# Performance work log

Hardware: AMD Instinct MI355X
Metric: run time of the kernel (lower is better)

## Reference

```python
import jax, jax.numpy as jnp
import numpy as np

T, N, G = 4, 100000, 128
R, B, K = 4, 4096, 32
I = 128


def setup_inputs() -> dict:
    key = jax.random.key(0)
    k1, k2, k3, k4 = jax.random.split(key, 4)
    embeddings = jax.random.normal(k1, (T, N, G), dtype=jnp.float32)
    neighbor_idx = jax.random.randint(k2, (T, R, B, K), 0, N, dtype=jnp.int32)
    neighbor_mask = jax.random.randint(k3, (T, R, B, K), 0, 2).astype(jnp.bool_)
    # xavier_uniform per relation weight [G, I]
    limit = float(np.sqrt(6.0 / (G + I)))
    weights = jax.random.uniform(k4, (R, G, I), dtype=jnp.float32, minval=-limit, maxval=limit)
    return {
        "embeddings": embeddings,
        "weights": weights,
        "neighbor_idx": neighbor_idx,
        "neighbor_mask": neighbor_mask,
        "train_year": T,
    }


def reference(embeddings, weights, neighbor_idx, neighbor_mask, train_year):
    # embeddings: [T, N, G]; neighbor_idx/mask: [T, R, B, K]; weights: [R, G, I]
    m = neighbor_mask.astype(embeddings.dtype)               # [T,R,B,K]
    year = jnp.arange(embeddings.shape[0])[:, None, None, None]
    gathered = embeddings[year, neighbor_idx]                 # [T,R,B,K,G]
    summed = jnp.einsum('trbkg,trbk->trbg', gathered, m)      # masked neighbor sum
    cnt = jnp.maximum(m.sum(-1), 1.0)                         # empty list -> divide by 1 (zeros row)
    mean = summed / cnt[..., None]                            # [T,R,B,G]
    out = jnp.einsum('trbg,rgi->tbi', mean, weights)          # per-relation matmul, sum over R
    return out.reshape(-1, train_year, weights.shape[-1])     # raw flat reshape, as in original
```

## Files before the change

### kernel.cpp

```cpp
#include <hip/hip_runtime.h>

#define T_ 4
#define N_ 100000
#define G_ 128
#define R_ 4
#define B_ 4096
#define K_ 32
#define I_ 128
#define BB 8

__global__ __launch_bounds__(128) void static_influence_kernel(
    const float* __restrict__ E,
    const float* __restrict__ W,
    const int*   __restrict__ idx,
    const int*   __restrict__ msk,
    float*       __restrict__ out)
{
    const int tid = threadIdx.x;
    const int blk = blockIdx.x;
    const int t  = blk / (B_ / BB);
    const int b0 = (blk % (B_ / BB)) * BB;

    __shared__ float mean_s[BB][G_];

    float acc[BB];
#pragma unroll
    for (int bb = 0; bb < BB; ++bb) acc[bb] = 0.f;

    const float* __restrict__ Et = E + (size_t)t * N_ * G_;

    for (int r = 0; r < R_; ++r) {
        for (int bb = 0; bb < BB; ++bb) {
            const int base = (((t * R_ + r) * B_) + (b0 + bb)) * K_;
            float s = 0.f;
            float cnt = 0.f;
#pragma unroll
            for (int k = 0; k < K_; ++k) {
                const int   id = idx[base + k];
                const float m  = (msk[base + k] != 0) ? 1.0f : 0.0f;
                s   += m * Et[(size_t)id * G_ + tid];
                cnt += m;
            }
            mean_s[bb][tid] = s / fmaxf(cnt, 1.0f);
        }
        __syncthreads();

        const float* __restrict__ Wr = W + r * G_ * I_;
#pragma unroll 8
        for (int g = 0; g < G_; ++g) {
            const float w = Wr[g * I_ + tid];
#pragma unroll
            for (int bb = 0; bb < BB; ++bb)
                acc[bb] += mean_s[bb][g] * w;
        }
        __syncthreads();
    }

#pragma unroll
    for (int bb = 0; bb < BB; ++bb)
        out[((size_t)t * B_ + (b0 + bb)) * I_ + tid] = acc[bb];
}

extern "C" void kernel_launch(void* const* d_in, const int* in_sizes, int n_in,
                              void* d_out, int out_size, void* d_ws, size_t ws_size,
                              hipStream_t stream) {
    const float* E   = (const float*)d_in[0];
    const float* W   = (const float*)d_in[1];
    const int*   idx = (const int*)d_in[2];
    const int*   msk = (const int*)d_in[3];
    float* out = (float*)d_out;

    dim3 grid(T_ * (B_ / BB));
    dim3 block(128);
    hipLaunchKernelGGL(static_influence_kernel, grid, block, 0, stream,
                       E, W, idx, msk, out);
}
```

Before: 399.3 us.

## Stage packed idx/mask in LDS and gather rows with float4 per half-wave

```diff
diff --git a/kernel.cpp b/kernel.cpp
--- a/kernel.cpp
+++ b/kernel.cpp
@@ -9,7 +9,7 @@
 #define I_ 128
 #define BB 8
 
-__global__ __launch_bounds__(128) void static_influence_kernel(
+__global__ __launch_bounds__(256) void static_influence_kernel(
     const float* __restrict__ E,
     const float* __restrict__ W,
     const int*   __restrict__ idx,
@@ -18,47 +18,76 @@
 {
     const int tid = threadIdx.x;
     const int blk = blockIdx.x;
-    const int t  = blk / (B_ / BB);
-    const int b0 = (blk % (B_ / BB)) * BB;
+    const int t   = blk / (B_ / BB);
+    const int b0  = (blk % (B_ / BB)) * BB;
 
     __shared__ float mean_s[BB][G_];
+    __shared__ int   idxm_s[BB * K_];
 
-    float acc[BB];
-#pragma unroll
-    for (int bb = 0; bb < BB; ++bb) acc[bb] = 0.f;
+    const int wave = tid >> 6;
+    const int lane = tid & 63;
+    const int half = lane >> 5;
+    const int gl   = lane & 31;
+    const int bbg  = 2 * wave + half;
+
+    const int iset = tid >> 7;
+    const int i    = tid & 127;
+
+    float acc0 = 0.f, acc1 = 0.f, acc2 = 0.f, acc3 = 0.f;
 
     const float* __restrict__ Et = E + (size_t)t * N_ * G_;
 
     for (int r = 0; r < R_; ++r) {
-        for (int bb = 0; bb < BB; ++bb) {
-            const int base = (((t * R_ + r) * B_) + (b0 + bb)) * K_;
-            float s = 0.f;
-            float cnt = 0.f;
-#pragma unroll
-            for (int k = 0; k < K_; ++k) {
-                const int   id = idx[base + k];
-                const float m  = (msk[base + k] != 0) ? 1.0f : 0.0f;
-                s   += m * Et[(size_t)id * G_ + tid];
-                cnt += m;
-            }
-            mean_s[bb][tid] = s / fmaxf(cnt, 1.0f);
+        {
+            const int base = ((t * R_ + r) * B_ + b0) * K_;
+            const int v = idx[base + tid];
+            const int m = msk[base + tid];
+            idxm_s[tid] = m ? (v | 0x80000000) : v;
         }
         __syncthreads();
 
+        float4 s4 = make_float4(0.f, 0.f, 0.f, 0.f);
+        float  cnt = 0.f;
+#pragma unroll 8
+        for (int k = 0; k < K_; ++k) {
+            const int   v  = idxm_s[bbg * K_ + k];
+            const int   id = v & 0x7FFFFFFF;
+            const float fm = (v < 0) ? 1.0f : 0.0f;
+            const float4 e4 = *reinterpret_cast<const float4*>(Et + (size_t)id * G_ + gl * 4);
+            s4.x += fm * e4.x;  s4.y += fm * e4.y;
+            s4.z += fm * e4.z;  s4.w += fm * e4.w;
+            cnt  += fm;
+        }
+        const float inv = 1.0f / fmaxf(cnt, 1.0f);
+        *reinterpret_cast<float4*>(&mean_s[bbg][gl * 4]) =
+            make_float4(s4.x * inv, s4.y * inv, s4.z * inv, s4.w * inv);
+        __syncthreads();
+
         const float* __restrict__ Wr = W + r * G_ * I_;
-#pragma unroll 8
-        for (int g = 0; g < G_; ++g) {
-            const float w = Wr[g * I_ + tid];
-#pragma unroll
-            for (int bb = 0; bb < BB; ++bb)
-                acc[bb] += mean_s[bb][g] * w;
+        const int bbm = iset * 4;
+#pragma unroll 2
+        for (int g = 0; g < G_; g += 4) {
+            const float w0 = Wr[(g + 0) * I_ + i];
+            const float w1 = Wr[(g + 1) * I_ + i];
+            const float w2 = Wr[(g + 2) * I_ + i];
+            const float w3 = Wr[(g + 3) * I_ + i];
+            const float4 m0 = *reinterpret_cast<const float4*>(&mean_s[bbm + 0][g]);
+            const float4 m1 = *reinterpret_cast<const float4*>(&mean_s[bbm + 1][g]);
+            const float4 m2 = *reinterpret_cast<const float4*>(&mean_s[bbm + 2][g]);
+            const float4 m3 = *reinterpret_cast<const float4*>(&mean_s[bbm + 3][g]);
+            acc0 += m0.x * w0 + m0.y * w1 + m0.z * w2 + m0.w * w3;
+            acc1 += m1.x * w0 + m1.y * w1 + m1.z * w2 + m1.w * w3;
+            acc2 += m2.x * w0 + m2.y * w1 + m2.z * w2 + m2.w * w3;
+            acc3 += m3.x * w0 + m3.y * w1 + m3.z * w2 + m3.w * w3;
         }
         __syncthreads();
     }
 
-#pragma unroll
-    for (int bb = 0; bb < BB; ++bb)
-        out[((size_t)t * B_ + (b0 + bb)) * I_ + tid] = acc[bb];
+    const size_t ob = ((size_t)t * B_ + b0 + iset * 4) * I_ + i;
+    out[ob + 0 * I_] = acc0;
+    out[ob + 1 * I_] = acc1;
+    out[ob + 2 * I_] = acc2;
+    out[ob + 3 * I_] = acc3;
 }
 
 extern "C" void kernel_launch(void* const* d_in, const int* in_sizes, int n_in,
@@ -71,7 +100,7 @@
     float* out = (float*)d_out;
 
     dim3 grid(T_ * (B_ / BB));
-    dim3 block(128);
+    dim3 block(256);
     hipLaunchKernelGGL(static_influence_kernel, grid, block, 0, stream,
                        E, W, idx, msk, out);
 }
```

New measurement: 392.6 us. Within noise of the previous version (-1.7%).
